# Kernel tuning notes

Measured on AMD Instinct MI355X. Metric: run time of the kernel, lower is better.

Reference implementation:

```python
import math
import jax, jax.numpy as jnp
import numpy as np

HEAD_SIZE = 64
DEPTH = 0

def lambda_init_fn(depth):
    depth = depth + 1
    return 0.8 - 0.6 * math.exp(-0.3 * depth)

def setup_inputs() -> dict:
    key = jax.random.key(0)
    ks = jax.random.split(key, 9)
    B, T, C = 4, 4096, 1024
    H2 = 2 * HEAD_SIZE  # 128
    return {
        "x":  jax.random.normal(ks[0], (B, T, C), dtype=jnp.float32),
        "Wq": jax.random.normal(ks[1], (C, H2), dtype=jnp.float32) * (C ** -0.5),
        "Wk": jax.random.normal(ks[2], (C, H2), dtype=jnp.float32) * (C ** -0.5),
        "Wv": jax.random.normal(ks[3], (C, H2), dtype=jnp.float32) * (C ** -0.5),
        "lambda_q1": jax.random.normal(ks[4], (HEAD_SIZE,), dtype=jnp.float32) * 0.1,
        "lambda_q2": jax.random.normal(ks[5], (HEAD_SIZE,), dtype=jnp.float32) * 0.1,
        "lambda_k1": jax.random.normal(ks[6], (HEAD_SIZE,), dtype=jnp.float32) * 0.1,
        "lambda_k2": jax.random.normal(ks[7], (HEAD_SIZE,), dtype=jnp.float32) * 0.1,
    }

def reference(x, Wq, Wk, Wv, lambda_q1, lambda_q2, lambda_k1, lambda_k2):
    B, T, C = x.shape
    q = x @ Wq  # (B,T,2*hs)
    k = x @ Wk
    v = x @ Wv  # (B,T,2*hs)
    q1, q2 = jnp.split(q, 2, axis=-1)
    k1, k2 = jnp.split(k, 2, axis=-1)
    scale = 1.0 / math.sqrt(HEAD_SIZE)
    w1 = jnp.einsum('btd,bsd->bts', q1, k1) * scale  # (B,T,T)
    w2 = jnp.einsum('btd,bsd->bts', q2, k2) * scale
    causal = jnp.tril(jnp.ones((T, T), dtype=bool))
    neg_inf = jnp.float32(-jnp.inf)
    w1 = jnp.where(causal, w1, neg_inf)
    w2 = jnp.where(causal, w2, neg_inf)
    lam1 = jnp.exp(jnp.sum(lambda_q1 * lambda_k1))
    lam2 = jnp.exp(jnp.sum(lambda_q2 * lambda_k2))
    lam = lam1 - lam2 + lambda_init_fn(DEPTH)
    weights = jax.nn.softmax(w1, axis=-1) - lam * jax.nn.softmax(w2, axis=-1)
    out = jnp.einsum('bts,bsd->btd', weights, v)  # (B,T,2*hs)
    return out
```

## Files before the change

### kernel.cpp

```cpp
#include <hip/hip_runtime.h>
#include <hip/hip_bf16.h>

typedef __bf16 bf16x8 __attribute__((ext_vector_type(8)));
typedef float f32x4 __attribute__((ext_vector_type(4)));

#define LOG2E 1.4426950408889634f
#define LAMBDA_INIT 0.3555090675909693f
#define CEXP 0.18033688011112042f
#define MOFF 11.541560327111708f

#define K_OFF   ((size_t)16384 * 128)
#define VT_OFF  ((size_t)2 * 16384 * 128)
#define PART_OFF_BYTES ((size_t)12582912)
#define WT_OFF_BYTES   ((size_t)46661632)
#define REC_FLOATS 4160

__device__ __forceinline__ unsigned short f2bf(float f) {
    __hip_bfloat16 h = __float2bfloat16(f);
    unsigned short u;
    __builtin_memcpy(&u, &h, 2);
    return u;
}
__device__ __forceinline__ float bf2f(unsigned short u) {
    unsigned int x = ((unsigned int)u) << 16;
    float f;
    __builtin_memcpy(&f, &x, 4);
    return f;
}
__device__ __forceinline__ unsigned int cvt_pk_bf16(float a, float b) {
    unsigned int r;
    asm volatile("v_cvt_pk_bf16_f32 %0, %1, %2" : "=v"(r) : "v"(a), "v"(b));
    return r;
}

__global__ __launch_bounds__(256) void prep_wt(
    const float* __restrict__ Wq, const float* __restrict__ Wk,
    const float* __restrict__ Wv, unsigned short* __restrict__ WT) {
    const int kt = blockIdx.x, nt = blockIdx.y, mat = blockIdx.z;
    const float* W = (mat == 0) ? Wq : (mat == 1) ? Wk : Wv;
    unsigned short* O = WT + (size_t)mat * 128 * 1024;
    __shared__ float tb[64][65];
    const int r = threadIdx.x >> 2, c4 = (threadIdx.x & 3) * 16;
    for (int j = 0; j < 4; ++j) {
        float4 v = *(const float4*)&W[(size_t)(kt * 64 + r) * 128 + nt * 64 + c4 + j * 4];
        tb[r][c4 + j * 4 + 0] = v.x;
        tb[r][c4 + j * 4 + 1] = v.y;
        tb[r][c4 + j * 4 + 2] = v.z;
        tb[r][c4 + j * 4 + 3] = v.w;
    }
    __syncthreads();
    unsigned short tmp[16];
    for (int j = 0; j < 16; ++j) tmp[j] = f2bf(tb[c4 + j][r]);
    *(uint4*)&O[(size_t)(nt * 64 + r) * 1024 + kt * 64 + c4] = *(uint4*)&tmp[0];
    *(uint4*)&O[(size_t)(nt * 64 + r) * 1024 + kt * 64 + c4 + 8] = *(uint4*)&tmp[8];
}

__global__ __launch_bounds__(256) void qkv_gemm(
    const float* __restrict__ x, const unsigned short* __restrict__ WT,
    unsigned short* __restrict__ qkv) {
    const int tid = threadIdx.x;
    const int l = tid & 63, wid = tid >> 6;
    const int g = l >> 4, i16 = l & 15;
    const int row0 = blockIdx.x * 128;
    const int mat = blockIdx.y;
    const unsigned short* Wt = WT + (size_t)mat * 128 * 1024;

    __shared__ unsigned short smem[2][128][72];
    auto xs = smem[0];
    auto wt = smem[1];

    f32x4 acc[2][8];
    const f32x4 z4 = {0.f, 0.f, 0.f, 0.f};
    for (int a = 0; a < 2; ++a)
        for (int b = 0; b < 8; ++b) acc[a][b] = z4;

    for (int k0 = 0; k0 < 1024; k0 += 64) {
        __syncthreads();
        {
            const int c = (tid & 15) * 4;
            const int rbase = tid >> 4;
            #pragma unroll
            for (int it = 0; it < 8; ++it) {
                int r = rbase + it * 16;
                const float4 v = *(const float4*)&x[(size_t)(row0 + r) * 1024 + k0 + c];
                ushort4 pk = make_ushort4(f2bf(v.x), f2bf(v.y), f2bf(v.z), f2bf(v.w));
                *(ushort4*)&xs[r][c] = pk;
            }
        }
        {
            #pragma unroll
            for (int it = 0; it < 4; ++it) {
                int lin = it * 256 + tid;
                int n = lin >> 3, k8 = (lin & 7) * 8;
                *(uint4*)&wt[n][k8] = *(const uint4*)&Wt[(size_t)n * 1024 + k0 + k8];
            }
        }
        __syncthreads();

        bf16x8 af[2][2];
        for (int rb = 0; rb < 2; ++rb)
            for (int c = 0; c < 2; ++c)
                af[rb][c] = *(const bf16x8*)&xs[wid * 32 + rb * 16 + i16][c * 32 + 8 * g];
        for (int nb = 0; nb < 8; ++nb) {
            bf16x8 b0 = *(const bf16x8*)&wt[nb * 16 + i16][8 * g];
            bf16x8 b1 = *(const bf16x8*)&wt[nb * 16 + i16][32 + 8 * g];
            for (int rb = 0; rb < 2; ++rb) {
                acc[rb][nb] = __builtin_amdgcn_mfma_f32_16x16x32_bf16(af[rb][0], b0, acc[rb][nb], 0, 0, 0);
                acc[rb][nb] = __builtin_amdgcn_mfma_f32_16x16x32_bf16(af[rb][1], b1, acc[rb][nb], 0, 0, 0);
            }
        }
    }

    __syncthreads();
    unsigned short(*ts)[136] = (unsigned short(*)[136]) & smem[0][0][0];
    for (int rb = 0; rb < 2; ++rb)
        for (int nb = 0; nb < 8; ++nb)
            for (int r = 0; r < 4; ++r)
                ts[wid * 32 + rb * 16 + g * 4 + r][nb * 16 + i16] = f2bf(acc[rb][nb][r]);
    __syncthreads();

    const int bq = row0 >> 12;
    const int s0b = (row0 & 4095) >> 6;
    if (mat == 0) {
        unsigned short* outp = qkv + (size_t)row0 * 128;
        #pragma unroll
        for (int it = 0; it < 8; ++it) {
            int tr = it * 16 + (tid >> 4), dv0 = (tid & 15) * 8;
            *(uint4*)&outp[tr * 128 + dv0] = *(const uint4*)&ts[tr][dv0];
        }
    } else if (mat == 1) {
        unsigned short* kimg = qkv + K_OFF;
        #pragma unroll
        for (int it = 0; it < 8; ++it) {
            int lin = it * 256 + tid;
            int tile = lin >> 10;
            int branch_ = (lin >> 9) & 1;
            int region = (lin >> 6) & 7;
            int slot = lin & 63;
            int row = tile * 64 + (region >> 1) * 16 + (slot & 15);
            int d = branch_ * 64 + (region & 1) * 32 + (slot >> 4) * 8;
            uint4 vv = *(const uint4*)&ts[row][d];
            size_t off = ((size_t)((bq * 64 + s0b + tile) * 2 + branch_) * 4096) + (region * 64 + slot) * 8;
            *(uint4*)&kimg[off] = vv;
        }
    } else {
        unsigned short* vimg = qkv + VT_OFF;
        #pragma unroll
        for (int it = 0; it < 8; ++it) {
            int lin = it * 256 + tid;
            int tile = lin >> 10;
            int rem = lin & 1023;
            int region = rem >> 6;
            int slot = rem & 63;
            int dv = (region >> 1) * 16 + (slot & 15);
            int kv0 = (region & 1) * 32 + (slot >> 4) * 8;
            unsigned short tmp[8];
            #pragma unroll
            for (int e = 0; e < 8; ++e) tmp[e] = ts[tile * 64 + kv0 + e][dv];
            size_t off = ((size_t)(bq * 64 + s0b + tile) * 8192) + (region * 64 + slot) * 8;
            *(uint4*)&vimg[off] = *(uint4*)tmp;
        }
    }
}

__global__ __launch_bounds__(256, 3) void diff_attn_pair(
    const unsigned short* __restrict__ q, const unsigned short* __restrict__ kimg,
    const unsigned short* __restrict__ vimg,
    float* __restrict__ part) {
    const int bx = blockIdx.x, b = blockIdx.y;
    const int c = blockIdx.z >> 1, branch = blockIdx.z & 1;
    const int bxe = (c & 1) ? (31 - bx) : bx;
    const int t_o = 63 - 2 * bxe, t_e = t_o - 1;
    const int n = t_o + 1;
    const int s_lo = (c * n) >> 2, smax = ((c + 1) * n) >> 2;

    const int tid = threadIdx.x;
    const int l = tid & 63, w = tid >> 6;
    const int gq = l >> 4, i16 = l & 15;
    const float NEGINF = -__builtin_inff();

    __shared__ unsigned short ksf[4096];
    __shared__ unsigned short psf[8192];

    float* recA = part + ((((size_t)b * 64 + t_e) * 4 + c) * 2 + branch) * REC_FLOATS;
    float* recB = part + ((((size_t)b * 64 + t_o) * 4 + c) * 2 + branch) * REC_FLOATS;

    if (s_lo >= smax) {
        unsigned int* pa_ = (unsigned int*)recA;
        unsigned int* pb_ = (unsigned int*)recB;
        for (int i = tid; i < REC_FLOATS; i += 256) { pa_[i] = 0u; pb_[i] = 0u; }
        return;
    }
    const bool emptyA = (s_lo > t_e);
    if (emptyA) {
        unsigned int* pa_ = (unsigned int*)recA;
        for (int i = tid; i < REC_FLOATS; i += 256) pa_[i] = 0u;
    }

    const size_t bbase = (size_t)b * 4096;
    const unsigned short* kimg_b = kimg + (size_t)b * 524288;
    const unsigned short* vimg_b = vimg + (size_t)b * 524288;
    const int tid8 = tid * 8;
    const int l8 = l * 8;
    const f32x4 z4 = {0.f, 0.f, 0.f, 0.f};

    bf16x8 qfA[2], qfB[2];
    #pragma unroll
    for (int cc = 0; cc < 2; ++cc) {
        qfA[cc] = *(const bf16x8*)&q[(bbase + t_e * 64 + w * 16 + i16) * 128 + branch * 64 + cc * 32 + 8 * gq];
        qfB[cc] = *(const bf16x8*)&q[(bbase + t_o * 64 + w * 16 + i16) * 128 + branch * 64 + cc * 32 + 8 * gq];
    }

    float lsumA = 0.f, lsumB = 0.f;
    f32x4 acc[2][4][2];
    for (int qs = 0; qs < 2; ++qs)
        for (int qg = 0; qg < 4; ++qg)
            for (int j = 0; j < 2; ++j) acc[qs][qg][j] = z4;

    int pdst[4];
    #pragma unroll
    for (int cb = 0; cb < 4; ++cb)
        pdst[cb] = ((w * 2 + (cb >> 1)) * 64 + ((cb & 1) * 2 + (gq >> 1)) * 16 + i16) * 8 + (gq & 1) * 4;

    uint4 kr0, kr1;
    bf16x8 vb00, vb01, vb10, vb11;

#define K_ISSUE(s_) do {                                                            \
        const unsigned short* kp = &kimg_b[((size_t)(s_) * 2 + branch) * 4096];     \
        kr0 = *(const uint4*)&kp[tid8];                                             \
        kr1 = *(const uint4*)&kp[tid8 + 2048];                                      \
    } while (0)
#define V_ISSUE(s_) do {                                                            \
        const unsigned short* vp = &vimg_b[(size_t)(s_) * 8192 + w * 2048];         \
        vb00 = *(const bf16x8*)&vp[l8];                                             \
        vb01 = *(const bf16x8*)&vp[512 + l8];                                       \
        vb10 = *(const bf16x8*)&vp[1024 + l8];                                      \
        vb11 = *(const bf16x8*)&vp[1536 + l8];                                      \
    } while (0)

    K_ISSUE(s_lo);
    V_ISSUE(s_lo);
    #pragma unroll 1
    for (int s = s_lo; s < smax; ++s) {
        __syncthreads();
        *(uint4*)&ksf[tid8] = kr0;
        *(uint4*)&ksf[tid8 + 2048] = kr1;
        if (s + 1 < smax) K_ISSUE(s + 1);
        __syncthreads();
        const bool aAct = (s != t_o);

        if (aAct) {
            f32x4 sc[4];
            for (int cb = 0; cb < 4; ++cb) sc[cb] = z4;
            __builtin_amdgcn_s_setprio(1);
            #pragma unroll
            for (int cb = 0; cb < 4; ++cb)
                for (int cc = 0; cc < 2; ++cc) {
                    bf16x8 kf = *(const bf16x8*)&ksf[((cb * 2 + cc) * 64 + l) * 8];
                    sc[cb] = __builtin_amdgcn_mfma_f32_16x16x32_bf16(kf, qfA[cc], sc[cb], 0, 0, 0);
                }
            __builtin_amdgcn_s_setprio(0);
            if (s == t_e) {
                int ql = w * 16 + i16;
                for (int cb = 0; cb < 4; ++cb)
                    for (int r = 0; r < 4; ++r)
                        if (cb * 16 + gq * 4 + r > ql) sc[cb][r] = NEGINF;
            }
            #pragma unroll
            for (int cb = 0; cb < 4; ++cb) {
                float p0 = exp2f(fmaf(sc[cb][0], CEXP, -MOFF));
                float p1 = exp2f(fmaf(sc[cb][1], CEXP, -MOFF));
                float p2 = exp2f(fmaf(sc[cb][2], CEXP, -MOFF));
                float p3 = exp2f(fmaf(sc[cb][3], CEXP, -MOFF));
                lsumA += (p0 + p1) + (p2 + p3);
                uint2 pw;
                pw.x = cvt_pk_bf16(p0, p1);
                pw.y = cvt_pk_bf16(p2, p3);
                *(uint2*)&psf[pdst[cb]] = pw;
            }
        }
        {
            f32x4 sc[4];
            for (int cb = 0; cb < 4; ++cb) sc[cb] = z4;
            __builtin_amdgcn_s_setprio(1);
            #pragma unroll
            for (int cb = 0; cb < 4; ++cb)
                for (int cc = 0; cc < 2; ++cc) {
                    bf16x8 kf = *(const bf16x8*)&ksf[((cb * 2 + cc) * 64 + l) * 8];
                    sc[cb] = __builtin_amdgcn_mfma_f32_16x16x32_bf16(kf, qfB[cc], sc[cb], 0, 0, 0);
                }
            __builtin_amdgcn_s_setprio(0);
            if (s == t_o) {
                int ql = w * 16 + i16;
                for (int cb = 0; cb < 4; ++cb)
                    for (int r = 0; r < 4; ++r)
                        if (cb * 16 + gq * 4 + r > ql) sc[cb][r] = NEGINF;
            }
            #pragma unroll
            for (int cb = 0; cb < 4; ++cb) {
                float p0 = exp2f(fmaf(sc[cb][0], CEXP, -MOFF));
                float p1 = exp2f(fmaf(sc[cb][1], CEXP, -MOFF));
                float p2 = exp2f(fmaf(sc[cb][2], CEXP, -MOFF));
                float p3 = exp2f(fmaf(sc[cb][3], CEXP, -MOFF));
                lsumB += (p0 + p1) + (p2 + p3);
                uint2 pw;
                pw.x = cvt_pk_bf16(p0, p1);
                pw.y = cvt_pk_bf16(p2, p3);
                *(uint2*)&psf[4096 + pdst[cb]] = pw;
            }
        }
        __syncthreads();

        __builtin_amdgcn_s_setprio(1);
        if (aAct) {
            #pragma unroll
            for (int qg = 0; qg < 4; ++qg) {
                bf16x8 pa0 = *(const bf16x8*)&psf[(qg * 2 + 0) * 512 + l8];
                bf16x8 pa1 = *(const bf16x8*)&psf[(qg * 2 + 1) * 512 + l8];
                acc[0][qg][0] = __builtin_amdgcn_mfma_f32_16x16x32_bf16(pa0, vb00, acc[0][qg][0], 0, 0, 0);
                acc[0][qg][0] = __builtin_amdgcn_mfma_f32_16x16x32_bf16(pa1, vb01, acc[0][qg][0], 0, 0, 0);
                acc[0][qg][1] = __builtin_amdgcn_mfma_f32_16x16x32_bf16(pa0, vb10, acc[0][qg][1], 0, 0, 0);
                acc[0][qg][1] = __builtin_amdgcn_mfma_f32_16x16x32_bf16(pa1, vb11, acc[0][qg][1], 0, 0, 0);
            }
        }
        #pragma unroll
        for (int qg = 0; qg < 4; ++qg) {
            bf16x8 pa0 = *(const bf16x8*)&psf[4096 + (qg * 2 + 0) * 512 + l8];
            bf16x8 pa1 = *(const bf16x8*)&psf[4096 + (qg * 2 + 1) * 512 + l8];
            acc[1][qg][0] = __builtin_amdgcn_mfma_f32_16x16x32_bf16(pa0, vb00, acc[1][qg][0], 0, 0, 0);
            acc[1][qg][0] = __builtin_amdgcn_mfma_f32_16x16x32_bf16(pa1, vb01, acc[1][qg][0], 0, 0, 0);
            acc[1][qg][1] = __builtin_amdgcn_mfma_f32_16x16x32_bf16(pa0, vb10, acc[1][qg][1], 0, 0, 0);
            acc[1][qg][1] = __builtin_amdgcn_mfma_f32_16x16x32_bf16(pa1, vb11, acc[1][qg][1], 0, 0, 0);
        }
        __builtin_amdgcn_s_setprio(0);
        if (s + 1 < smax) V_ISSUE(s + 1);
    }
#undef K_ISSUE
#undef V_ISSUE

    lsumA += __shfl_xor(lsumA, 16);
    lsumA += __shfl_xor(lsumA, 32);
    lsumB += __shfl_xor(lsumB, 16);
    lsumB += __shfl_xor(lsumB, 32);
    if (!emptyA) {
        if (gq == 0) recA[w * 16 + i16] = lsumA;
        unsigned short* OA = (unsigned short*)(recA + 64);
        for (int qg = 0; qg < 4; ++qg)
            for (int j = 0; j < 2; ++j)
                for (int r = 0; r < 4; ++r)
                    OA[(qg * 16 + gq * 4 + r) * 128 + (w * 2 + j) * 16 + i16] = f2bf(acc[0][qg][j][r]);
    }
    {
        if (gq == 0) recB[w * 16 + i16] = lsumB;
        unsigned short* OB = (unsigned short*)(recB + 64);
        for (int qg = 0; qg < 4; ++qg)
            for (int j = 0; j < 2; ++j)
                for (int r = 0; r < 4; ++r)
                    OB[(qg * 16 + gq * 4 + r) * 128 + (w * 2 + j) * 16 + i16] = f2bf(acc[1][qg][j][r]);
    }
}

__global__ __launch_bounds__(256) void diff_combine(
    const float* __restrict__ part,
    const float* __restrict__ lq1, const float* __restrict__ lq2,
    const float* __restrict__ lk1, const float* __restrict__ lk2,
    float* __restrict__ out) {
    const int t = blockIdx.x, b = blockIdx.y;
    const int tid = threadIdx.x;
    __shared__ float sl[2][64];
    __shared__ float s_lam;

    const float* recbase = part + (((size_t)b * 64 + t) * 4) * 2 * REC_FLOATS;

    if (tid < 64) {
        float s1 = lq1[tid] * lk1[tid];
        float s2 = lq2[tid] * lk2[tid];
        for (int off = 32; off > 0; off >>= 1) {
            s1 += __shfl_xor(s1, off);
            s2 += __shfl_xor(s2, off);
        }
        if (tid == 0) s_lam = expf(s1) - expf(s2) + LAMBDA_INIT;
    }
    if (tid < 128) {
        int r = tid & 63, br = tid >> 6;
        float acc = 0.f;
        for (int c = 0; c < 4; ++c) acc += recbase[(c * 2 + br) * REC_FLOATS + r];
        sl[br][r] = acc;
    }
    __syncthreads();
    const float lam = s_lam;

    float* op = out + ((size_t)b * 4096 + (size_t)t * 64) * 128;
    for (int grp = 0; grp < 4; ++grp) {
        int gid = grp * 256 + tid;
        int e = gid * 8;
        int row = e >> 7;
        float o1[8] = {0, 0, 0, 0, 0, 0, 0, 0}, o2[8] = {0, 0, 0, 0, 0, 0, 0, 0};
        #pragma unroll
        for (int c = 0; c < 4; ++c) {
            const unsigned short* O0 = (const unsigned short*)(recbase + (c * 2 + 0) * REC_FLOATS + 64);
            const unsigned short* O1 = (const unsigned short*)(recbase + (c * 2 + 1) * REC_FLOATS + 64);
            uint4 u0 = *(const uint4*)&O0[e];
            uint4 u1 = *(const uint4*)&O1[e];
            const unsigned short* e0 = (const unsigned short*)&u0;
            const unsigned short* e1 = (const unsigned short*)&u1;
            #pragma unroll
            for (int j = 0; j < 8; ++j) {
                o1[j] += bf2f(e0[j]);
                o2[j] += bf2f(e1[j]);
            }
        }
        float l1inv = 1.0f / sl[0][row], l2inv = 1.0f / sl[1][row];
        float res[8];
        #pragma unroll
        for (int j = 0; j < 8; ++j) res[j] = o1[j] * l1inv - lam * o2[j] * l2inv;
        *(float4*)&op[e] = *(float4*)&res[0];
        *(float4*)&op[e + 4] = *(float4*)&res[4];
    }
}

extern "C" void kernel_launch(void* const* d_in, const int* in_sizes, int n_in,
                              void* d_out, int out_size, void* d_ws, size_t ws_size,
                              hipStream_t stream) {
    const float* x   = (const float*)d_in[0];
    const float* Wq  = (const float*)d_in[1];
    const float* Wk  = (const float*)d_in[2];
    const float* Wv  = (const float*)d_in[3];
    const float* lq1 = (const float*)d_in[4];
    const float* lq2 = (const float*)d_in[5];
    const float* lk1 = (const float*)d_in[6];
    const float* lk2 = (const float*)d_in[7];
    float* out = (float*)d_out;
    unsigned short* qkv = (unsigned short*)d_ws;
    float* part = (float*)((char*)d_ws + PART_OFF_BYTES);
    unsigned short* WT = (unsigned short*)((char*)d_ws + WT_OFF_BYTES);

    prep_wt<<<dim3(16, 2, 3), 256, 0, stream>>>(Wq, Wk, Wv, WT);
    qkv_gemm<<<dim3(128, 3), 256, 0, stream>>>(x, WT, qkv);

    const unsigned short* qb = qkv;
    const unsigned short* kb = qkv + K_OFF;
    const unsigned short* vtb = qkv + VT_OFF;
    diff_attn_pair<<<dim3(32, 4, 8), 256, 0, stream>>>(qb, kb, vtb, part);
    diff_combine<<<dim3(64, 4), 256, 0, stream>>>(part, lq1, lq2, lk1, lk2, out);
}
```

Baseline: 98.42 us.

## Raise KV split count to eight when workspace allows and skip zero-filling empty chunks

Makes the number of KV-sequence chunks per query tile a runtime parameter and picks eight chunks when the workspace is large enough, otherwise four. This doubles the attention grid so more blocks fill the GPU's compute units and the causal load is balanced more evenly. Empty chunks now return early without zero-filling their partial records, and the combine kernel works out which chunks are valid and skips the rest. In exchange the combine step reads more partial records and the partial buffer in the workspace grows.

```diff
diff --git a/kernel.cpp b/kernel.cpp
--- a/kernel.cpp
+++ b/kernel.cpp
@@ -12,7 +12,6 @@
 #define K_OFF   ((size_t)16384 * 128)
 #define VT_OFF  ((size_t)2 * 16384 * 128)
 #define PART_OFF_BYTES ((size_t)12582912)
-#define WT_OFF_BYTES   ((size_t)46661632)
 #define REC_FLOATS 4160
 
 __device__ __forceinline__ unsigned short f2bf(float f) {
@@ -166,13 +165,15 @@
 __global__ __launch_bounds__(256, 3) void diff_attn_pair(
     const unsigned short* __restrict__ q, const unsigned short* __restrict__ kimg,
     const unsigned short* __restrict__ vimg,
-    float* __restrict__ part) {
+    float* __restrict__ part, int ncs) {
     const int bx = blockIdx.x, b = blockIdx.y;
     const int c = blockIdx.z >> 1, branch = blockIdx.z & 1;
     const int bxe = (c & 1) ? (31 - bx) : bx;
     const int t_o = 63 - 2 * bxe, t_e = t_o - 1;
     const int n = t_o + 1;
-    const int s_lo = (c * n) >> 2, smax = ((c + 1) * n) >> 2;
+    const int s_lo = (c * n) >> ncs, smax = ((c + 1) * n) >> ncs;
+
+    if (s_lo >= smax) return;
 
     const int tid = threadIdx.x;
     const int l = tid & 63, w = tid >> 6;
@@ -182,20 +183,9 @@
     __shared__ unsigned short ksf[4096];
     __shared__ unsigned short psf[8192];
 
-    float* recA = part + ((((size_t)b * 64 + t_e) * 4 + c) * 2 + branch) * REC_FLOATS;
-    float* recB = part + ((((size_t)b * 64 + t_o) * 4 + c) * 2 + branch) * REC_FLOATS;
-
-    if (s_lo >= smax) {
-        unsigned int* pa_ = (unsigned int*)recA;
-        unsigned int* pb_ = (unsigned int*)recB;
-        for (int i = tid; i < REC_FLOATS; i += 256) { pa_[i] = 0u; pb_[i] = 0u; }
-        return;
-    }
+    float* recA = part + ((((size_t)(b * 64 + t_e) << ncs) + c) * 2 + branch) * REC_FLOATS;
+    float* recB = part + ((((size_t)(b * 64 + t_o) << ncs) + c) * 2 + branch) * REC_FLOATS;
     const bool emptyA = (s_lo > t_e);
-    if (emptyA) {
-        unsigned int* pa_ = (unsigned int*)recA;
-        for (int i = tid; i < REC_FLOATS; i += 256) pa_[i] = 0u;
-    }
 
     const size_t bbase = (size_t)b * 4096;
     const unsigned short* kimg_b = kimg + (size_t)b * 524288;
@@ -364,13 +354,15 @@
     const float* __restrict__ part,
     const float* __restrict__ lq1, const float* __restrict__ lq2,
     const float* __restrict__ lk1, const float* __restrict__ lk2,
-    float* __restrict__ out) {
+    float* __restrict__ out, int ncs) {
     const int t = blockIdx.x, b = blockIdx.y;
     const int tid = threadIdx.x;
+    const int nc = 1 << ncs;
+    const int n = (t | 1) + 1;
     __shared__ float sl[2][64];
     __shared__ float s_lam;
 
-    const float* recbase = part + (((size_t)b * 64 + t) * 4) * 2 * REC_FLOATS;
+    const float* recbase = part + (((size_t)(b * 64 + t) << ncs)) * 2 * REC_FLOATS;
 
     if (tid < 64) {
         float s1 = lq1[tid] * lk1[tid];
@@ -384,7 +376,11 @@
     if (tid < 128) {
         int r = tid & 63, br = tid >> 6;
         float acc = 0.f;
-        for (int c = 0; c < 4; ++c) acc += recbase[(c * 2 + br) * REC_FLOATS + r];
+        for (int c = 0; c < nc; ++c) {
+            int lo = (c * n) >> ncs, hi = ((c + 1) * n) >> ncs;
+            if (lo >= hi || lo > t) continue;
+            acc += recbase[(c * 2 + br) * REC_FLOATS + r];
+        }
         sl[br][r] = acc;
     }
     __syncthreads();
@@ -396,8 +392,9 @@
         int e = gid * 8;
         int row = e >> 7;
         float o1[8] = {0, 0, 0, 0, 0, 0, 0, 0}, o2[8] = {0, 0, 0, 0, 0, 0, 0, 0};
-        #pragma unroll
-        for (int c = 0; c < 4; ++c) {
+        for (int c = 0; c < nc; ++c) {
+            int lo = (c * n) >> ncs, hi = ((c + 1) * n) >> ncs;
+            if (lo >= hi || lo > t) continue;
             const unsigned short* O0 = (const unsigned short*)(recbase + (c * 2 + 0) * REC_FLOATS + 64);
             const unsigned short* O1 = (const unsigned short*)(recbase + (c * 2 + 1) * REC_FLOATS + 64);
             uint4 u0 = *(const uint4*)&O0[e];
@@ -432,8 +429,16 @@
     const float* lk2 = (const float*)d_in[7];
     float* out = (float*)d_out;
     unsigned short* qkv = (unsigned short*)d_ws;
+
+    const size_t WT_BYTES = (size_t)3 * 128 * 1024 * 2;
+    int ncs = 2;
+    {
+        size_t part8 = (size_t)256 * 8 * 2 * REC_FLOATS * 4;
+        if (ws_size >= PART_OFF_BYTES + part8 + WT_BYTES) ncs = 3;
+    }
+    const size_t part_bytes = (size_t)256 * (1 << ncs) * 2 * REC_FLOATS * 4;
     float* part = (float*)((char*)d_ws + PART_OFF_BYTES);
-    unsigned short* WT = (unsigned short*)((char*)d_ws + WT_OFF_BYTES);
+    unsigned short* WT = (unsigned short*)((char*)d_ws + PART_OFF_BYTES + part_bytes);
 
     prep_wt<<<dim3(16, 2, 3), 256, 0, stream>>>(Wq, Wk, Wv, WT);
     qkv_gemm<<<dim3(128, 3), 256, 0, stream>>>(x, WT, qkv);
@@ -441,6 +446,6 @@
     const unsigned short* qb = qkv;
     const unsigned short* kb = qkv + K_OFF;
     const unsigned short* vtb = qkv + VT_OFF;
-    diff_attn_pair<<<dim3(32, 4, 8), 256, 0, stream>>>(qb, kb, vtb, part);
-    diff_combine<<<dim3(64, 4), 256, 0, stream>>>(part, lq1, lq2, lk1, lk2, out);
-}
+    diff_attn_pair<<<dim3(32, 4, 2 << ncs), 256, 0, stream>>>(qb, kb, vtb, part, ncs);
+    diff_combine<<<dim3(64, 4), 256, 0, stream>>>(part, lq1, lq2, lk1, lk2, out, ncs);
+}
```

After: 102.2 us. +3.8%, slower.
